# Optimization experiments

Hardware: AMD Instinct MI355X
Metric: run time of the kernel (lower is better)

## Reference

```python
import jax, jax.numpy as jnp
import numpy as np

B = 64          # decode batch (one token per sequence)
HID = 4096      # hidden_size
HQ = 32         # num query heads
HKV = 8         # num kv heads (GQA, groups = 4)
D = 128         # head_dim
BS = 16         # block_size of paged KV cache
MAXB = 64       # max blocks per sequence -> max context 1024
MAXPOS = 4096   # rope table length
TOTAL_SLOTS = B * MAXB * BS


def setup_inputs() -> dict:
    key = jax.random.key(0)
    ks = jax.random.split(key, 10)
    hidden = jax.random.normal(ks[0], (B, 1, HID), jnp.float32)
    context_lens = jax.random.randint(ks[1], (B,), 512, BS * MAXB + 1).astype(jnp.int32)
    positions = (context_lens - 1).reshape(B, 1)  # decoding token position
    # each sequence owns a contiguous range of blocks
    block_tables = jnp.arange(B * MAXB, dtype=jnp.int32).reshape(B, MAXB)
    last = context_lens - 1
    slot_mapping = (block_tables[jnp.arange(B), last // BS] * BS + last % BS).astype(jnp.int32)
    inv_freq = 1.0 / (10000.0 ** (jnp.arange(0, D, 2, dtype=jnp.float32) / D))
    freqs = jnp.outer(jnp.arange(MAXPOS, dtype=jnp.float32), inv_freq)  # [MAXPOS, D/2]
    cos, sin = jnp.cos(freqs), jnp.sin(freqs)
    key_cache = jax.random.normal(ks[2], (TOTAL_SLOTS, HKV, D), jnp.float32) * 0.5
    value_cache = jax.random.normal(ks[3], (TOTAL_SLOTS, HKV, D), jnp.float32) * 0.5
    Wq = jax.random.normal(ks[4], (HQ * D, HID), jnp.float32) * 0.02
    Wk = jax.random.normal(ks[5], (HKV * D, HID), jnp.float32) * 0.02
    Wv = jax.random.normal(ks[6], (HKV * D, HID), jnp.float32) * 0.02
    Wo = jax.random.normal(ks[7], (HID, HQ * D), jnp.float32) * 0.02
    return dict(hidden=hidden, positions=positions, cos=cos, sin=sin,
                key_cache=key_cache, value_cache=value_cache,
                slot_mapping=slot_mapping, block_tables=block_tables,
                context_lens=context_lens, Wq=Wq, Wk=Wk, Wv=Wv, Wo=Wo)


def reference(hidden, positions, cos, sin, key_cache, value_cache,
              slot_mapping, block_tables, context_lens, Wq, Wk, Wv, Wo):
    b, s, _ = hidden.shape  # s == 1 (paged decode path)
    q = (hidden @ Wq.T).reshape(b, s, HQ, D)
    k = (hidden @ Wk.T).reshape(b, s, HKV, D)
    v = (hidden @ Wv.T).reshape(b, s, HKV, D)
    # rotary embedding (half-split convention)
    c = cos[positions][:, :, None, :]  # [b,s,1,D/2]
    sn = sin[positions][:, :, None, :]
    def rope(x):
        x1, x2 = jnp.split(x, 2, axis=-1)
        return jnp.concatenate([x1 * c - x2 * sn, x2 * c + x1 * sn], axis=-1)
    q, k = rope(q), rope(k)
    # scatter current token's K/V into the paged cache via slot_mapping
    kc = key_cache.at[slot_mapping].set(k.reshape(-1, HKV, D))
    vc = value_cache.at[slot_mapping].set(v.reshape(-1, HKV, D))
    # gather each sequence's KV via block tables
    T = MAXB * BS
    t = jnp.arange(T)
    slots = block_tables[:, t // BS] * BS + (t % BS)  # [b, T]
    keys = kc[slots]   # [b, T, HKV, D]
    vals = vc[slots]   # [b, T, HKV, D]
    # GQA attention, q has one token per sequence
    G = HQ // HKV
    qg = q.reshape(b, HKV, G, D)
    scores = jnp.einsum('bkgd,btkd->bkgt', qg, keys) / jnp.sqrt(jnp.float32(D))
    mask = t[None, :] < context_lens[:, None]  # [b, T]
    scores = jnp.where(mask[:, None, None, :], scores, -jnp.inf)
    p = jax.nn.softmax(scores, axis=-1)
    out = jnp.einsum('bkgt,btkd->bkgd', p, vals).reshape(b, 1, HQ * D)
    return out @ Wo.T
```

## Files before the change

### kernel.cpp

```cpp
#include <hip/hip_runtime.h>
#include <hip/hip_bf16.h>

#define B_    64
#define HID_  4096
#define HQ_   32
#define HKV_  8
#define D_    128
#define BS_   16
#define MAXB_ 64

#define KS      16
#define KCHUNK  (HID_ / KS)
#define QKV_ROWS 6144
#define O_ROWS   4096
#define SPLITS  8

#define REGION_SZ ((size_t)KS * QKV_ROWS * 64)
#define QKVF_SZ  ((size_t)64 * 6144)
#define XB_SZ    ((size_t)HID_ * 64)

typedef __attribute__((ext_vector_type(8))) short bf16x8;
typedef __attribute__((ext_vector_type(4))) float f32x4;

__device__ inline unsigned short f2bf(float x) {
  __hip_bfloat16 h = __float2bfloat16(x);
  union { __hip_bfloat16 b; unsigned short u; } v; v.b = h;
  return v.u;
}
__device__ inline float bf2f(unsigned short h) {
  union { float f; unsigned u; } v; v.u = ((unsigned)h) << 16;
  return v.f;
}

__global__ __launch_bounds__(256) void convert_x(
    const float* __restrict__ X, unsigned short* __restrict__ XBhi,
    unsigned short* __restrict__ XBlo)
{
  int idx = blockIdx.x * 256 + threadIdx.x;
  int kg = idx >> 6, b = idx & 63;
  const float* xp = X + (size_t)b * HID_ + kg * 8;
  float4 a = *(const float4*)xp, c = *(const float4*)(xp + 4);
  float xs[8] = {a.x, a.y, a.z, a.w, c.x, c.y, c.z, c.w};
  unsigned short hi[8], lo[8];
  #pragma unroll
  for (int j = 0; j < 8; ++j) {
    hi[j] = f2bf(xs[j]);
    lo[j] = f2bf(xs[j] - bf2f(hi[j]));
  }
  *(uint4*)(XBhi + (size_t)idx * 8) = *(const uint4*)hi;
  *(uint4*)(XBlo + (size_t)idx * 8) = *(const uint4*)lo;
}

__global__ __launch_bounds__(256, 4) void gemm_mfma(
    const float* __restrict__ W0, const float* __restrict__ W1,
    const float* __restrict__ W2,
    const unsigned short* __restrict__ XBhi,
    const unsigned short* __restrict__ XBlo,
    int split1, int split2, int rows_total, float* __restrict__ part)
{
  const int tid = threadIdx.x;
  const int l   = tid & 63;
  const int w   = tid >> 6;
  const int r0  = blockIdx.x * 128 + w * 32;
  const int k0  = blockIdx.y * KCHUNK;

  const float* W; int rloc;
  if (r0 < split1)      { W = W0; rloc = r0; }
  else if (r0 < split2) { W = W1; rloc = r0 - split1; }
  else                  { W = W2; rloc = r0 - split2; }

  const int lm = l & 15;
  const int lk = l >> 4;

  const float* wp0 = W + (size_t)(rloc + lm) * HID_ + k0 + lk * 8;
  const float* wp1 = wp0 + (size_t)16 * HID_;
  const unsigned short* bh = XBhi + ((size_t)(k0 / 8 + lk) * 64 + lm) * 8;
  const unsigned short* bl = XBlo + ((size_t)(k0 / 8 + lk) * 64 + lm) * 8;

  f32x4 acc[2][4];
  #pragma unroll
  for (int rt = 0; rt < 2; ++rt)
    #pragma unroll
    for (int ct = 0; ct < 4; ++ct)
      #pragma unroll
      for (int i = 0; i < 4; ++i) acc[rt][ct][i] = 0.f;

  #pragma unroll 2
  for (int ks = 0; ks < KCHUNK / 32; ++ks) {
    bf16x8 Bh[4], Bl[4];
    #pragma unroll
    for (int ct = 0; ct < 4; ++ct) {
      Bh[ct] = *(const bf16x8*)(bh + (size_t)ks * 2048 + ct * 128);
      Bl[ct] = *(const bf16x8*)(bl + (size_t)ks * 2048 + ct * 128);
    }
    #pragma unroll
    for (int rt = 0; rt < 2; ++rt) {
      const float* wp = (rt ? wp1 : wp0) + ks * 32;
      float4 a0 = *(const float4*)wp;
      float4 a1 = *(const float4*)(wp + 4);
      float xs[8] = {a0.x, a0.y, a0.z, a0.w, a1.x, a1.y, a1.z, a1.w};
      bf16x8 Ah, Al;
      #pragma unroll
      for (int j = 0; j < 8; ++j) {
        unsigned short h = f2bf(xs[j]);
        Ah[j] = (short)h;
        Al[j] = (short)f2bf(xs[j] - bf2f(h));
      }
      #pragma unroll
      for (int ct = 0; ct < 4; ++ct) {
        acc[rt][ct] = __builtin_amdgcn_mfma_f32_16x16x32_bf16(Ah, Bh[ct], acc[rt][ct], 0, 0, 0);
        acc[rt][ct] = __builtin_amdgcn_mfma_f32_16x16x32_bf16(Al, Bh[ct], acc[rt][ct], 0, 0, 0);
        acc[rt][ct] = __builtin_amdgcn_mfma_f32_16x16x32_bf16(Ah, Bl[ct], acc[rt][ct], 0, 0, 0);
      }
    }
  }

  #pragma unroll
  for (int rt = 0; rt < 2; ++rt)
    #pragma unroll
    for (int ct = 0; ct < 4; ++ct) {
      int row = r0 + rt * 16 + lk * 4;
      int bat = ct * 16 + lm;
      #pragma unroll
      for (int i = 0; i < 4; ++i)
        part[((size_t)blockIdx.y * rows_total + row + i) * 64 + bat] = acc[rt][ct][i];
    }
}

__global__ __launch_bounds__(256) void reduce_rope(
    const float* __restrict__ part, const float* __restrict__ cosT,
    const float* __restrict__ sinT, const int* __restrict__ positions,
    float* __restrict__ qkvf)
{
  const int bb  = threadIdx.x & 63;
  const int cid = blockIdx.x * 4 + (threadIdx.x >> 6);
  const int pos = positions[bb];

  if (cid < 2048) {
    const int hq = cid >> 6, d0 = cid & 63;
    const int r1 = hq * 128 + d0;
    float x1 = 0.f, x2 = 0.f;
    #pragma unroll 8
    for (int ks = 0; ks < KS; ++ks) {
      x1 += part[((size_t)ks * QKV_ROWS + r1) * 64 + bb];
      x2 += part[((size_t)ks * QKV_ROWS + r1 + 64) * 64 + bb];
    }
    float c = cosT[pos * 64 + d0], s = sinT[pos * 64 + d0];
    const float scale = 0.08838834764831843f;
    qkvf[(size_t)(bb * 32 + hq) * 128 + d0]      = (x1 * c - x2 * s) * scale;
    qkvf[(size_t)(bb * 32 + hq) * 128 + d0 + 64] = (x2 * c + x1 * s) * scale;
  } else if (cid < 2560) {
    const int c2 = cid - 2048;
    const int kh = c2 >> 6, d0 = c2 & 63;
    const int r1 = 4096 + kh * 128 + d0;
    float x1 = 0.f, x2 = 0.f;
    #pragma unroll 8
    for (int ks = 0; ks < KS; ++ks) {
      x1 += part[((size_t)ks * QKV_ROWS + r1) * 64 + bb];
      x2 += part[((size_t)ks * QKV_ROWS + r1 + 64) * 64 + bb];
    }
    float c = cosT[pos * 64 + d0], s = sinT[pos * 64 + d0];
    qkvf[262144 + (size_t)(bb * 8 + kh) * 128 + d0]      = x1 * c - x2 * s;
    qkvf[262144 + (size_t)(bb * 8 + kh) * 128 + d0 + 64] = x2 * c + x1 * s;
  } else {
    const int c2 = cid - 2560;
    const int kh = c2 >> 6, d0 = c2 & 63;
    const int r1 = 5120 + kh * 128 + d0;
    float x1 = 0.f, x2 = 0.f;
    #pragma unroll 8
    for (int ks = 0; ks < KS; ++ks) {
      x1 += part[((size_t)ks * QKV_ROWS + r1) * 64 + bb];
      x2 += part[((size_t)ks * QKV_ROWS + r1 + 64) * 64 + bb];
    }
    qkvf[327680 + (size_t)(bb * 8 + kh) * 128 + d0]      = x1;
    qkvf[327680 + (size_t)(bb * 8 + kh) * 128 + d0 + 64] = x2;
  }
}

__global__ __launch_bounds__(256, 4) void attn_split(
    const float* __restrict__ qkvf, const float* __restrict__ kcache,
    const float* __restrict__ vcache, const int* __restrict__ btab,
    const int* __restrict__ ctxlen,
    float* __restrict__ part_o,
    float* __restrict__ part_ml)
{
  const int bid = blockIdx.x;
  const int s   = bid & (SPLITS - 1);
  const int bh  = bid >> 3;
  const int b = bh >> 3, h = bh & 7;
  const int ctx   = ctxlen[b];
  const int chunk = (ctx + SPLITS - 1) / SPLITS;
  const int t0 = s * chunk;
  const int t1 = min(ctx, t0 + chunk);
  const int last = ctx - 1;
  const int tEnd = min(t1, last);

  const int tid  = threadIdx.x;
  const int half = tid >> 5;
  const int d4   = tid & 31;

  __shared__ int   sblk[16];
  __shared__ float wm[4][4], wl[4][4];
  __shared__ float wacc[4][4][128];

  const int blk0 = t0 >> 4;
  if (tid < 16) {
    int ib = blk0 + tid;
    sblk[tid] = (ib < MAXB_) ? btab[b * MAXB_ + ib] : 0;
  }
  __syncthreads();

  float4 qf[4];
  #pragma unroll
  for (int g = 0; g < 4; ++g)
    qf[g] = *(const float4*)(qkvf + (size_t)(b * 32 + h * 4 + g) * 128 + d4 * 4);

  float m[4], l[4], acc[4][4];
  #pragma unroll
  for (int g = 0; g < 4; ++g) {
    m[g] = -1e30f; l[g] = 0.f;
    #pragma unroll
    for (int j = 0; j < 4; ++j) acc[g][j] = 0.f;
  }

  for (int t = t0 + half; t < tEnd; t += 8) {
    int slot = sblk[(t >> 4) - blk0] * BS_ + (t & 15);
    const float* base = kcache + ((size_t)slot * HKV_ + h) * D_ + d4 * 4;
    const float* vbas = vcache + ((size_t)slot * HKV_ + h) * D_ + d4 * 4;
    float4 kv = *(const float4*)base;
    float4 vv = *(const float4*)vbas;

    float p0 = qf[0].x * kv.x + qf[0].y * kv.y + qf[0].z * kv.z + qf[0].w * kv.w;
    float p1 = qf[1].x * kv.x + qf[1].y * kv.y + qf[1].z * kv.z + qf[1].w * kv.w;
    float p2 = qf[2].x * kv.x + qf[2].y * kv.y + qf[2].z * kv.z + qf[2].w * kv.w;
    float p3 = qf[3].x * kv.x + qf[3].y * kv.y + qf[3].z * kv.z + qf[3].w * kv.w;
    #pragma unroll
    for (int mm = 16; mm >= 1; mm >>= 1) {
      p0 += __shfl_xor(p0, mm);
      p1 += __shfl_xor(p1, mm);
      p2 += __shfl_xor(p2, mm);
      p3 += __shfl_xor(p3, mm);
    }
    float pg[4] = {p0, p1, p2, p3};
    #pragma unroll
    for (int g = 0; g < 4; ++g) {
      float nm = fmaxf(m[g], pg[g]);
      float sc = __expf(m[g] - nm);
      float pe = __expf(pg[g] - nm);
      l[g] = l[g] * sc + pe;
      acc[g][0] = acc[g][0] * sc + pe * vv.x;
      acc[g][1] = acc[g][1] * sc + pe * vv.y;
      acc[g][2] = acc[g][2] * sc + pe * vv.z;
      acc[g][3] = acc[g][3] * sc + pe * vv.w;
      m[g] = nm;
    }
  }

  if (t1 > last && half == ((last - t0) & 7)) {
    const float* kp = qkvf + 262144 + (size_t)(b * 8 + h) * 128 + d4 * 4;
    const float* vp = qkvf + 327680 + (size_t)(b * 8 + h) * 128 + d4 * 4;
    float4 kv = *(const float4*)kp;
    float4 vv = *(const float4*)vp;
    float p0 = qf[0].x * kv.x + qf[0].y * kv.y + qf[0].z * kv.z + qf[0].w * kv.w;
    float p1 = qf[1].x * kv.x + qf[1].y * kv.y + qf[1].z * kv.z + qf[1].w * kv.w;
    float p2 = qf[2].x * kv.x + qf[2].y * kv.y + qf[2].z * kv.z + qf[2].w * kv.w;
    float p3 = qf[3].x * kv.x + qf[3].y * kv.y + qf[3].z * kv.z + qf[3].w * kv.w;
    #pragma unroll
    for (int mm = 16; mm >= 1; mm >>= 1) {
      p0 += __shfl_xor(p0, mm);
      p1 += __shfl_xor(p1, mm);
      p2 += __shfl_xor(p2, mm);
      p3 += __shfl_xor(p3, mm);
    }
    float pg[4] = {p0, p1, p2, p3};
    #pragma unroll
    for (int g = 0; g < 4; ++g) {
      float nm = fmaxf(m[g], pg[g]);
      float sc = __expf(m[g] - nm);
      float pe = __expf(pg[g] - nm);
      l[g] = l[g] * sc + pe;
      acc[g][0] = acc[g][0] * sc + pe * vv.x;
      acc[g][1] = acc[g][1] * sc + pe * vv.y;
      acc[g][2] = acc[g][2] * sc + pe * vv.z;
      acc[g][3] = acc[g][3] * sc + pe * vv.w;
      m[g] = nm;
    }
  }

  #pragma unroll
  for (int g = 0; g < 4; ++g) {
    float om = __shfl_xor(m[g], 32);
    float ol = __shfl_xor(l[g], 32);
    float M  = fmaxf(m[g], om);
    float s0 = __expf(m[g] - M);
    float s1 = __expf(om - M);
    l[g] = l[g] * s0 + ol * s1;
    #pragma unroll
    for (int j = 0; j < 4; ++j) {
      float oa = __shfl_xor(acc[g][j], 32);
      acc[g][j] = acc[g][j] * s0 + oa * s1;
    }
    m[g] = M;
  }
  if ((tid & 32) == 0) {
    int wv = tid >> 6;
    if (d4 == 0) {
      #pragma unroll
      for (int g = 0; g < 4; ++g) { wm[wv][g] = m[g]; wl[wv][g] = l[g]; }
    }
    #pragma unroll
    for (int g = 0; g < 4; ++g)
      #pragma unroll
      for (int j = 0; j < 4; ++j)
        wacc[wv][g][d4 * 4 + j] = acc[g][j];
  }
  __syncthreads();

  for (int idx = tid; idx < 512; idx += 256) {
    int g = idx >> 7, d = idx & 127;
    float M4 = fmaxf(fmaxf(wm[0][g], wm[1][g]), fmaxf(wm[2][g], wm[3][g]));
    float e0 = __expf(wm[0][g] - M4), e1 = __expf(wm[1][g] - M4);
    float e2 = __expf(wm[2][g] - M4), e3 = __expf(wm[3][g] - M4);
    float num = wacc[0][g][d] * e0 + wacc[1][g][d] * e1
              + wacc[2][g][d] * e2 + wacc[3][g][d] * e3;
    part_o[(size_t)bid * 512 + idx] = num;
    if (d == 0) {
      float lt = wl[0][g] * e0 + wl[1][g] * e1 + wl[2][g] * e2 + wl[3][g] * e3;
      part_ml[(size_t)bid * 8 + g * 2]     = M4;
      part_ml[(size_t)bid * 8 + g * 2 + 1] = lt;
    }
  }
}

__global__ __launch_bounds__(256) void attn_combine_xb(
    const float* __restrict__ part_o, const float* __restrict__ part_ml,
    unsigned short* __restrict__ XBhi, unsigned short* __restrict__ XBlo)
{
  const int bh = blockIdx.x;
  const int b = bh >> 3, h = bh & 7;
  const int tid = threadIdx.x;

  __shared__ float Sg[SPLITS][4];
  __shared__ float Dg[4];

  if (tid < 32) {
    int s = tid >> 2, g = tid & 3;
    float m = part_ml[((size_t)bh * SPLITS + s) * 8 + g * 2];
    float l = part_ml[((size_t)bh * SPLITS + s) * 8 + g * 2 + 1];
    float M = m;
    #pragma unroll
    for (int k = 4; k <= 16; k <<= 1) M = fmaxf(M, __shfl_xor(M, k));
    float scl = __expf(m - M);
    float dl = l * scl;
    #pragma unroll
    for (int k = 4; k <= 16; k <<= 1) dl += __shfl_xor(dl, k);
    Sg[s][g] = scl;
    if (s == 0) Dg[g] = dl;
  }
  __syncthreads();

  for (int idx = tid; idx < 512; idx += 256) {
    int g = idx >> 7, d = idx & 127;
    float num = 0.f;
    #pragma unroll
    for (int s = 0; s < SPLITS; ++s)
      num += Sg[s][g] * part_o[((size_t)bh * SPLITS + s) * 512 + idx];
    float val = num / Dg[g];
    int col = (h * 4 + g) * 128 + d;
    int kg = col >> 3, j = col & 7;
    unsigned short hi = f2bf(val);
    unsigned short lo = f2bf(val - bf2f(hi));
    XBhi[((size_t)kg * 64 + b) * 8 + j] = hi;
    XBlo[((size_t)kg * 64 + b) * 8 + j] = lo;
  }
}

__global__ __launch_bounds__(256) void reduce_out_t(
    const float* __restrict__ part, float* __restrict__ out)
{
  __shared__ float t[64][65];
  const int i0 = blockIdx.x * 64;
  const int lane = threadIdx.x & 63, q = threadIdx.x >> 6;

  #pragma unroll
  for (int rr = q; rr < 64; rr += 4) {
    float s = 0.f;
    #pragma unroll 8
    for (int ks = 0; ks < KS; ++ks)
      s += part[((size_t)ks * O_ROWS + i0 + rr) * 64 + lane];
    t[rr][lane] = s;
  }
  __syncthreads();
  #pragma unroll
  for (int rr = q; rr < 64; rr += 4)
    out[(size_t)rr * O_ROWS + i0 + lane] = t[lane][rr];
}

extern "C" void kernel_launch(void* const* d_in, const int* in_sizes, int n_in,
                              void* d_out, int out_size, void* d_ws, size_t ws_size,
                              hipStream_t stream)
{
  (void)in_sizes; (void)n_in; (void)out_size; (void)ws_size;
  const float* hidden    = (const float*)d_in[0];
  const int*   positions = (const int*)d_in[1];
  const float* cosT      = (const float*)d_in[2];
  const float* sinT      = (const float*)d_in[3];
  const float* kcache    = (const float*)d_in[4];
  const float* vcache    = (const float*)d_in[5];
  const int*   btab      = (const int*)d_in[7];
  const int*   ctx       = (const int*)d_in[8];
  const float* Wq        = (const float*)d_in[9];
  const float* Wk        = (const float*)d_in[10];
  const float* Wv        = (const float*)d_in[11];
  const float* Wo        = (const float*)d_in[12];
  float* out = (float*)d_out;

  float* ws      = (float*)d_ws;
  float* region  = ws;
  float* qkvf    = region + REGION_SZ;
  unsigned short* XBhi = (unsigned short*)(qkvf + QKVF_SZ);
  unsigned short* XBlo = XBhi + XB_SZ;
  float* part1   = region;
  float* part_o  = region;
  float* part_ml = region + (size_t)B_ * HKV_ * SPLITS * 512;
  float* part3   = region;

  convert_x<<<128, 256, 0, stream>>>(hidden, XBhi, XBlo);
  gemm_mfma<<<dim3(QKV_ROWS / 128, KS), 256, 0, stream>>>(
      Wq, Wk, Wv, XBhi, XBlo, 4096, 5120, QKV_ROWS, part1);
  reduce_rope<<<768, 256, 0, stream>>>(part1, cosT, sinT, positions, qkvf);
  attn_split<<<B_ * HKV_ * SPLITS, 256, 0, stream>>>(
      qkvf, kcache, vcache, btab, ctx, part_o, part_ml);
  attn_combine_xb<<<B_ * HKV_, 256, 0, stream>>>(part_o, part_ml, XBhi, XBlo);
  gemm_mfma<<<dim3(O_ROWS / 128, KS), 256, 0, stream>>>(
      Wo, Wo, Wo, XBhi, XBlo, O_ROWS, O_ROWS, O_ROWS, part3);
  reduce_out_t<<<O_ROWS / 64, 256, 0, stream>>>(part3, out);
}
```

Measured before the change: 183.5 us.

## Stage weight tile through swizzled LDS with coalesced loads in gemm_mfma

The GEMM now loads a 64-row by 256-column fp32 weight tile into a 64 KB shared buffer using fully coalesced float4 loads, all issued up front, with an XOR swizzle to avoid bank conflicts. MFMA fragments are then read from LDS instead of through strided per-lane global loads. Each block now covers 64 rows instead of 128, so the grid doubles, and occupancy is lowered to 2 blocks per SM because of the LDS use. The aim is better DRAM coalescing and more memory-level parallelism for this weight-bandwidth-bound decode GEMM. The cost is more LDS traffic, a sync, and 16 float4 staging registers per thread.

```diff
diff --git a/kernel.cpp b/kernel.cpp
--- a/kernel.cpp
+++ b/kernel.cpp
@@ -51,17 +51,19 @@
   *(uint4*)(XBlo + (size_t)idx * 8) = *(const uint4*)lo;
 }
 
-__global__ __launch_bounds__(256, 4) void gemm_mfma(
+__global__ __launch_bounds__(256, 2) void gemm_mfma(
     const float* __restrict__ W0, const float* __restrict__ W1,
     const float* __restrict__ W2,
     const unsigned short* __restrict__ XBhi,
     const unsigned short* __restrict__ XBlo,
     int split1, int split2, int rows_total, float* __restrict__ part)
 {
+  __shared__ float Abuf[64 * 256];
+
   const int tid = threadIdx.x;
   const int l   = tid & 63;
   const int w   = tid >> 6;
-  const int r0  = blockIdx.x * 128 + w * 32;
+  const int r0  = blockIdx.x * 64;
   const int k0  = blockIdx.y * KCHUNK;
 
   const float* W; int rloc;
@@ -69,62 +71,74 @@
   else if (r0 < split2) { W = W1; rloc = r0 - split1; }
   else                  { W = W2; rloc = r0 - split2; }
 
+  const float* Wb = W + (size_t)rloc * HID_ + k0;
+
+  float4 st[16];
+  #pragma unroll
+  for (int c = 0; c < 16; ++c) {
+    int idx = c * 256 + tid;
+    int row = idx >> 6, q = idx & 63;
+    st[c] = *(const float4*)(Wb + (size_t)row * HID_ + q * 4);
+  }
+  #pragma unroll
+  for (int c = 0; c < 16; ++c) {
+    int idx = c * 256 + tid;
+    int row = idx >> 6, q = idx & 63;
+    int qs = q ^ (row & 7);
+    *(float4*)&Abuf[row * 256 + qs * 4] = st[c];
+  }
+  __syncthreads();
+
   const int lm = l & 15;
   const int lk = l >> 4;
-
-  const float* wp0 = W + (size_t)(rloc + lm) * HID_ + k0 + lk * 8;
-  const float* wp1 = wp0 + (size_t)16 * HID_;
+  const int r  = w * 16 + lm;
+  const int rx = r & 7;
+  const float* arow = &Abuf[r * 256];
+
   const unsigned short* bh = XBhi + ((size_t)(k0 / 8 + lk) * 64 + lm) * 8;
   const unsigned short* bl = XBlo + ((size_t)(k0 / 8 + lk) * 64 + lm) * 8;
 
-  f32x4 acc[2][4];
-  #pragma unroll
-  for (int rt = 0; rt < 2; ++rt)
-    #pragma unroll
-    for (int ct = 0; ct < 4; ++ct)
-      #pragma unroll
-      for (int i = 0; i < 4; ++i) acc[rt][ct][i] = 0.f;
-
-  #pragma unroll 2
-  for (int ks = 0; ks < KCHUNK / 32; ++ks) {
+  f32x4 acc[4];
+  #pragma unroll
+  for (int ct = 0; ct < 4; ++ct)
+    #pragma unroll
+    for (int i = 0; i < 4; ++i) acc[ct][i] = 0.f;
+
+  #pragma unroll
+  for (int ks = 0; ks < 8; ++ks) {
     bf16x8 Bh[4], Bl[4];
     #pragma unroll
     for (int ct = 0; ct < 4; ++ct) {
       Bh[ct] = *(const bf16x8*)(bh + (size_t)ks * 2048 + ct * 128);
       Bl[ct] = *(const bf16x8*)(bl + (size_t)ks * 2048 + ct * 128);
     }
-    #pragma unroll
-    for (int rt = 0; rt < 2; ++rt) {
-      const float* wp = (rt ? wp1 : wp0) + ks * 32;
-      float4 a0 = *(const float4*)wp;
-      float4 a1 = *(const float4*)(wp + 4);
-      float xs[8] = {a0.x, a0.y, a0.z, a0.w, a1.x, a1.y, a1.z, a1.w};
-      bf16x8 Ah, Al;
-      #pragma unroll
-      for (int j = 0; j < 8; ++j) {
-        unsigned short h = f2bf(xs[j]);
-        Ah[j] = (short)h;
-        Al[j] = (short)f2bf(xs[j] - bf2f(h));
-      }
-      #pragma unroll
-      for (int ct = 0; ct < 4; ++ct) {
-        acc[rt][ct] = __builtin_amdgcn_mfma_f32_16x16x32_bf16(Ah, Bh[ct], acc[rt][ct], 0, 0, 0);
-        acc[rt][ct] = __builtin_amdgcn_mfma_f32_16x16x32_bf16(Al, Bh[ct], acc[rt][ct], 0, 0, 0);
-        acc[rt][ct] = __builtin_amdgcn_mfma_f32_16x16x32_bf16(Ah, Bl[ct], acc[rt][ct], 0, 0, 0);
-      }
-    }
-  }
-
-  #pragma unroll
-  for (int rt = 0; rt < 2; ++rt)
+    int g0 = ks * 8 + lk * 2;
+    float4 a0 = *(const float4*)&arow[(g0 ^ rx) * 4];
+    float4 a1 = *(const float4*)&arow[((g0 + 1) ^ rx) * 4];
+    float xs[8] = {a0.x, a0.y, a0.z, a0.w, a1.x, a1.y, a1.z, a1.w};
+    bf16x8 Ah, Al;
+    #pragma unroll
+    for (int j = 0; j < 8; ++j) {
+      unsigned short h = f2bf(xs[j]);
+      Ah[j] = (short)h;
+      Al[j] = (short)f2bf(xs[j] - bf2f(h));
+    }
     #pragma unroll
     for (int ct = 0; ct < 4; ++ct) {
-      int row = r0 + rt * 16 + lk * 4;
-      int bat = ct * 16 + lm;
-      #pragma unroll
-      for (int i = 0; i < 4; ++i)
-        part[((size_t)blockIdx.y * rows_total + row + i) * 64 + bat] = acc[rt][ct][i];
-    }
+      acc[ct] = __builtin_amdgcn_mfma_f32_16x16x32_bf16(Ah, Bh[ct], acc[ct], 0, 0, 0);
+      acc[ct] = __builtin_amdgcn_mfma_f32_16x16x32_bf16(Al, Bh[ct], acc[ct], 0, 0, 0);
+      acc[ct] = __builtin_amdgcn_mfma_f32_16x16x32_bf16(Ah, Bl[ct], acc[ct], 0, 0, 0);
+    }
+  }
+
+  #pragma unroll
+  for (int ct = 0; ct < 4; ++ct) {
+    int row = r0 + w * 16 + lk * 4;
+    int bat = ct * 16 + lm;
+    #pragma unroll
+    for (int i = 0; i < 4; ++i)
+      part[((size_t)blockIdx.y * rows_total + row + i) * 64 + bat] = acc[ct][i];
+  }
 }
 
 __global__ __launch_bounds__(256) void reduce_rope(
@@ -426,13 +440,13 @@
   float* part3   = region;
 
   convert_x<<<128, 256, 0, stream>>>(hidden, XBhi, XBlo);
-  gemm_mfma<<<dim3(QKV_ROWS / 128, KS), 256, 0, stream>>>(
+  gemm_mfma<<<dim3(QKV_ROWS / 64, KS), 256, 0, stream>>>(
       Wq, Wk, Wv, XBhi, XBlo, 4096, 5120, QKV_ROWS, part1);
   reduce_rope<<<768, 256, 0, stream>>>(part1, cosT, sinT, positions, qkvf);
   attn_split<<<B_ * HKV_ * SPLITS, 256, 0, stream>>>(
       qkvf, kcache, vcache, btab, ctx, part_o, part_ml);
   attn_combine_xb<<<B_ * HKV_, 256, 0, stream>>>(part_o, part_ml, XBhi, XBlo);
-  gemm_mfma<<<dim3(O_ROWS / 128, KS), 256, 0, stream>>>(
+  gemm_mfma<<<dim3(O_ROWS / 64, KS), 256, 0, stream>>>(
       Wo, Wo, Wo, XBhi, XBlo, O_ROWS, O_ROWS, O_ROWS, part3);
   reduce_out_t<<<O_ROWS / 64, 256, 0, stream>>>(part3, out);
 }
```

After: 200.6 us. 9.3% more time.
